# Optimization experiments

Hardware: AMD Instinct MI355X
Metric: run time of the kernel (lower is better)

## Reference

```python
import jax, jax.numpy as jnp
import numpy as np

NUM_HEADS = 16
NUM_HIDDENS = 1024
D_K = NUM_HIDDENS // NUM_HEADS
NEG_INF = -1.0e9


def setup_inputs() -> dict:
    key = jax.random.key(0)
    kx, kq, kk, kv, ko, kl = jax.random.split(key, 6)
    B, S, D = 2, 2048, NUM_HIDDENS
    scale = 1.0 / np.sqrt(D)
    return {
        "X": jax.random.normal(kx, (B, S, D), dtype=jnp.float32),
        "valid_lens": jax.random.randint(kl, (B,), 0, S, dtype=jnp.int64),
        "W_q": jax.random.normal(kq, (D, D), dtype=jnp.float32) * scale,
        "W_k": jax.random.normal(kk, (D, D), dtype=jnp.float32) * scale,
        "W_v": jax.random.normal(kv, (D, D), dtype=jnp.float32) * scale,
        "W_o": jax.random.normal(ko, (D, D), dtype=jnp.float32) * scale,
    }


def _split_heads(x):
    # [B, S, D] -> [B, H, S, d_k]
    B, S, _ = x.shape
    return x.reshape(B, S, NUM_HEADS, D_K).transpose(0, 2, 1, 3)


def reference(X, valid_lens, W_q, W_k, W_v, W_o):
    B, S, D = X.shape
    # nn.Linear(bias=False): y = x @ W.T  (W is [out, in])
    Q = _split_heads(jnp.einsum("bsd,ed->bse", X, W_q))  # [B,H,S,dk]
    K = _split_heads(jnp.einsum("bsd,ed->bse", X, W_k))
    V = _split_heads(jnp.einsum("bsd,ed->bse", X, W_v))

    scores = jnp.einsum("bhqd,bhkd->bhqk", Q, K) / jnp.sqrt(
        jnp.asarray(D_K, dtype=X.dtype)
    )  # [B,H,S,S]

    # key-position mask per batch: positions >= valid_len get -1e9
    mask = jnp.arange(S)[None, :] >= valid_lens[:, None]  # [B,S]
    scores = jnp.where(mask[:, None, None, :], jnp.asarray(NEG_INF, X.dtype), scores)

    attn = jax.nn.softmax(scores, axis=-1)  # dropout p=0 -> identity
    out = jnp.einsum("bhqk,bhkd->bhqd", attn, V)  # [B,H,S,dk]
    out = out.transpose(0, 2, 1, 3).reshape(B, S, D)
    return jnp.einsum("bsd,ed->bse", out, W_o)
```

## Files before the change

kernel.cpp:

```cpp
#include <hip/hip_runtime.h>
#include <stdint.h>

#define S_LEN 2048
#define BATCH 2
#define DMODEL 1024
#define NHEAD 16
#define DK 64
#define MROWS (BATCH * S_LEN)

typedef __attribute__((ext_vector_type(8))) short bf16x8;
typedef __attribute__((ext_vector_type(4))) float f32x4;
typedef __attribute__((ext_vector_type(4))) short short4v;
typedef __attribute__((ext_vector_type(2))) uint32_t u32x2;

__device__ __forceinline__ short f2b(float f) {
    union { float f; uint32_t u; } c; c.f = f;
    uint32_t u = c.u;
    return (short)((u + 0x7fffu + ((u >> 16) & 1u)) >> 16);
}

__device__ __forceinline__ void gload16(const void* g, void* l) {
    __builtin_amdgcn_global_load_lds(
        (const __attribute__((address_space(1))) void*)g,
        (__attribute__((address_space(3))) void*)l, 16, 0, 0);
}

__global__ void cvt_kernel(const float* __restrict__ X, const float* __restrict__ Wq,
                           const float* __restrict__ Wk, const float* __restrict__ Wv,
                           const float* __restrict__ Wo,
                           short* __restrict__ Xb, short* __restrict__ Wqb,
                           short* __restrict__ Wkb, short* __restrict__ Wvb,
                           short* __restrict__ Wob) {
    const float* src; short* dst; int n4;
    switch (blockIdx.y) {
        case 0:  src = X;  dst = Xb;  n4 = MROWS * DMODEL / 4;  break;
        case 1:  src = Wq; dst = Wqb; n4 = DMODEL * DMODEL / 4; break;
        case 2:  src = Wk; dst = Wkb; n4 = DMODEL * DMODEL / 4; break;
        case 3:  src = Wv; dst = Wvb; n4 = DMODEL * DMODEL / 4; break;
        default: src = Wo; dst = Wob; n4 = DMODEL * DMODEL / 4; break;
    }
    for (int i = blockIdx.x * blockDim.x + threadIdx.x; i < n4;
         i += gridDim.x * blockDim.x) {
        float4 v = ((const float4*)src)[i];
        short4v o;
        o[0] = f2b(v.x); o[1] = f2b(v.y); o[2] = f2b(v.z); o[3] = f2b(v.w);
        ((short4v*)dst)[i] = o;
    }
}

template <int OUT_F32>
__global__ __launch_bounds__(256) void gemm_bt(
    const short* __restrict__ A,
    const short* __restrict__ Bt0, const short* __restrict__ Bt1,
    const short* __restrict__ Bt2,
    short* __restrict__ Cb0, short* __restrict__ Cb1, short* __restrict__ Cb2,
    float* __restrict__ Cf, int M, int N, int K) {
    __shared__ short sA[2][128 * 32];
    __shared__ short sB[2][128 * 32];

    const short* Bt = Bt0;
    short* Cb = Cb0;
    if (blockIdx.z == 1) { Bt = Bt1; Cb = Cb1; }
    else if (blockIdx.z == 2) { Bt = Bt2; Cb = Cb2; }

    const int tid = threadIdx.x;
    const int lane = tid & 63;
    const int wid = tid >> 6;
    const int wr = wid >> 1, wc = wid & 1;
    const int brow = blockIdx.y * 128;
    const int bcol = blockIdx.x * 128;
    const int lr = lane & 15;
    const int kh = (lane >> 4) << 3;
    const int swg = ((lr >> 1) & 3) << 3;
    const int khs = kh ^ swg;

    f32x4 acc[4][4] = {};

    const int idx0 = tid, idx1 = tid + 256;
    const int ar0 = idx0 >> 2, ak0 = ((idx0 & 3) << 3) ^ (((ar0 >> 1) & 3) << 3);
    const int ar1 = idx1 >> 2, ak1 = ((idx1 & 3) << 3) ^ (((ar1 >> 1) & 3) << 3);

    const short* gA0 = A + (size_t)(brow + ar0) * K + ak0;
    const short* gA1 = A + (size_t)(brow + ar1) * K + ak1;
    const short* gB0 = Bt + (size_t)(bcol + ar0) * K + ak0;
    const short* gB1 = Bt + (size_t)(bcol + ar1) * K + ak1;

    const int nk = K >> 5;
    gload16(gA0, &sA[0][idx0 * 8]);
    gload16(gA1, &sA[0][idx1 * 8]);
    gload16(gB0, &sB[0][idx0 * 8]);
    gload16(gB1, &sB[0][idx1 * 8]);
    __syncthreads();

    int cur = 0;
    for (int kt = 0; kt < nk; ++kt) {
        if (kt + 1 < nk) {
            const int k0 = (kt + 1) << 5;
            gload16(gA0 + k0, &sA[cur ^ 1][idx0 * 8]);
            gload16(gA1 + k0, &sA[cur ^ 1][idx1 * 8]);
            gload16(gB0 + k0, &sB[cur ^ 1][idx0 * 8]);
            gload16(gB1 + k0, &sB[cur ^ 1][idx1 * 8]);
        }

        bf16x8 a[4], b[4];
#pragma unroll
        for (int mt = 0; mt < 4; ++mt)
            a[mt] = *(const bf16x8*)&sA[cur][(wr * 64 + mt * 16 + lr) * 32 + khs];
#pragma unroll
        for (int nt = 0; nt < 4; ++nt)
            b[nt] = *(const bf16x8*)&sB[cur][(wc * 64 + nt * 16 + lr) * 32 + khs];
        __builtin_amdgcn_s_setprio(1);
#pragma unroll
        for (int mt = 0; mt < 4; ++mt)
#pragma unroll
            for (int nt = 0; nt < 4; ++nt)
                acc[mt][nt] = __builtin_amdgcn_mfma_f32_16x16x32_bf16(
                    a[mt], b[nt], acc[mt][nt], 0, 0, 0);
        __builtin_amdgcn_s_setprio(0);

        __syncthreads();
        cur ^= 1;
    }

    const int rbase = (lane >> 4) << 2;
    const bool vtrans = (!OUT_F32) && (blockIdx.z == 2);
#pragma unroll
    for (int mt = 0; mt < 4; ++mt) {
#pragma unroll
        for (int nt = 0; nt < 4; ++nt) {
            if (vtrans) {
                int row0 = brow + wr * 64 + mt * 16 + rbase;
                int col = bcol + wc * 64 + nt * 16 + lr;
                int bb = row0 >> 11, key = row0 & 2047;
                int hh = col >> 6, d = col & 63;
                short4v pk;
#pragma unroll
                for (int j = 0; j < 4; ++j) pk[j] = f2b(acc[mt][nt][j]);
                *(short4v*)&Cb[((size_t)((bb * 16 + hh) * 64 + d)) * S_LEN + key] = pk;
            } else {
#pragma unroll
                for (int j = 0; j < 4; ++j) {
                    int row = brow + wr * 64 + mt * 16 + rbase + j;
                    int col = bcol + wc * 64 + nt * 16 + lr;
                    if (OUT_F32)
                        Cf[(size_t)row * N + col] = acc[mt][nt][j];
                    else
                        Cb[(size_t)row * N + col] = f2b(acc[mt][nt][j]);
                }
            }
        }
    }
}

__global__ __launch_bounds__(256) void attn_kernel(
    const short* __restrict__ Q, const short* __restrict__ K,
    const short* __restrict__ Vt, short* __restrict__ O,
    const int* __restrict__ vlens) {
    __shared__ short sK[2][64 * 64];
    __shared__ short sV[2][64 * 64];
    __shared__ short sP[4][2][16 * 64];

    const int tid = threadIdx.x;
    const int lane = tid & 63;
    const int w = tid >> 6;
    const int id = blockIdx.x;
    const int id2 = ((id & 7) << 6) | (id >> 3);
    const int qb = id2 & 15;
    const int bhx = id2 >> 4;
    const int b = bhx & 1, h = bhx >> 1;
    const int lr = lane & 15;
    const int kh = (lane >> 4) << 3;
    const int rbase = (lane >> 4) << 2;
    const int swq = (lr & 7) << 3;

    int vl = vlens[b];
    if (vl < 0) vl = 0;
    if (vl > S_LEN) vl = S_LEN;
    const bool allm = (vl == 0);
    if (allm) vl = S_LEN;
    const int nT = (vl + 63) >> 6;
    const int nFull = ((vl & 63) == 0) ? nT : nT - 1;

    const size_t rowbase = (size_t)(b * S_LEN) * DMODEL + h * DK;
    const short* vt = Vt + ((size_t)((b * 16 + h) * 64)) * S_LEN;

    const short* qrowA = Q + rowbase + (size_t)(qb * 128 + w * 32 + lr) * DMODEL;
    const short* qrowB = qrowA + 16 * DMODEL;
    bf16x8 qf0a = *(const bf16x8*)(qrowA + kh);
    bf16x8 qf1a = *(const bf16x8*)(qrowA + 32 + kh);
    bf16x8 qf0b = *(const bf16x8*)(qrowB + kh);
    bf16x8 qf1b = *(const bf16x8*)(qrowB + 32 + kh);
    if (allm) {
#pragma unroll
        for (int i = 0; i < 8; ++i) { qf0a[i] = 0; qf1a[i] = 0; qf0b[i] = 0; qf1b[i] = 0; }
    }

    f32x4 oacA[4] = {}, oacB[4] = {};
    float mA = -1e30f, mcA = -1e30f, lA = 0.f;
    float mB = -1e30f, mcB = -1e30f, lB = 0.f;
    const float CEXP = 0.18033688011112042f;
    const float THRADD = 44.361419556f;

    const int lofs0 = lr * 64 + (kh ^ swq);
    const int lofs1 = lr * 64 + ((32 + kh) ^ swq);

    const int kr0 = tid >> 3;
    const int kr1 = kr0 + 32;
    const int kc0 = (((tid & 7) ^ (kr0 & 7)) << 3);
    const int kc1 = (((tid & 7) ^ (kr1 & 7)) << 3);

    const short* kA = K + rowbase + (size_t)kr0 * DMODEL + kc0;
    const short* kB = K + rowbase + (size_t)kr1 * DMODEL + kc1;
    const short* vA = vt + (size_t)kr0 * S_LEN + kc0;
    const short* vB = vt + (size_t)kr1 * S_LEN + kc1;

    gload16(kA, &sK[0][tid * 8]);
    gload16(kB, &sK[0][(tid + 256) * 8]);
    gload16(vA, &sV[0][tid * 8]);
    gload16(vB, &sV[0][(tid + 256) * 8]);
    __syncthreads();

#define SOFTMAX_FRAG(SACC, MRUN, MC, LRUN, OAC, SPW)                            \
    do {                                                                        \
        float t0 = fmaxf(fmaxf(SACC[0][0], SACC[0][1]), SACC[0][2]);            \
        float t1 = fmaxf(fmaxf(SACC[0][3], SACC[1][0]), SACC[1][1]);            \
        float t2 = fmaxf(fmaxf(SACC[1][2], SACC[1][3]), SACC[2][0]);            \
        float t3 = fmaxf(fmaxf(SACC[2][1], SACC[2][2]), SACC[2][3]);            \
        float t4 = fmaxf(fmaxf(SACC[3][0], SACC[3][1]), SACC[3][2]);            \
        float pmax = fmaxf(fmaxf(fmaxf(t0, t1), t2),                            \
                           fmaxf(fmaxf(t3, t4), SACC[3][3]));                   \
        if (__any(pmax > MRUN + THRADD)) {                                      \
            float mx = pmax;                                                    \
            mx = fmaxf(mx, __shfl_xor(mx, 16));                                 \
            mx = fmaxf(mx, __shfl_xor(mx, 32));                                 \
            float scl = __builtin_exp2f((MRUN - mx) * CEXP);                    \
            MRUN = mx;                                                          \
            MC = mx * CEXP;                                                     \
            LRUN *= scl;                                                        \
            _Pragma("unroll")                                                   \
            for (int dt = 0; dt < 4; ++dt)                                      \
                _Pragma("unroll")                                               \
                for (int j = 0; j < 4; ++j) OAC[dt][j] *= scl;                  \
        }                                                                       \
        float p[16];                                                            \
        _Pragma("unroll")                                                       \
        for (int nt = 0; nt < 4; ++nt)                                          \
            _Pragma("unroll")                                                   \
            for (int j = 0; j < 4; ++j)                                         \
                p[nt * 4 + j] = __builtin_exp2f(                                \
                    __builtin_fmaf(SACC[nt][j], CEXP, -MC));                    \
        float ls = ((p[0] + p[1]) + (p[2] + p[3])) +                            \
                   ((p[4] + p[5]) + (p[6] + p[7]));                             \
        ls += ((p[8] + p[9]) + (p[10] + p[11])) +                               \
              ((p[12] + p[13]) + (p[14] + p[15]));                              \
        LRUN += ls;                                                             \
        _Pragma("unroll")                                                       \
        for (int nt = 0; nt < 4; ++nt) {                                        \
            u32x2 r;                                                            \
            asm("v_cvt_pk_bf16_f32 %0, %1, %2"                                  \
                : "=v"(r[0]) : "v"(p[nt * 4 + 0]), "v"(p[nt * 4 + 1]));         \
            asm("v_cvt_pk_bf16_f32 %0, %1, %2"                                  \
                : "=v"(r[1]) : "v"(p[nt * 4 + 2]), "v"(p[nt * 4 + 3]));         \
            *(u32x2*)&SPW[lr * 64 + ((nt * 16 + rbase) ^ swq)] = r;             \
        }                                                                       \
    } while (0)

#define TILE_BODY(MASKED_C)                                                     \
    do {                                                                        \
        constexpr bool MASKED = MASKED_C;                                       \
        const short* sKc = sK[cur];                                             \
        const short* sVc = sV[cur];                                             \
        const short* kL0 = sKc + lofs0;                                         \
        const short* kL1 = sKc + lofs1;                                         \
        f32x4 saccA[4] = {}, saccB[4] = {};                                     \
        __builtin_amdgcn_s_setprio(1);                                          \
        _Pragma("unroll")                                                       \
        for (int nt = 0; nt < 4; ++nt) {                                        \
            bf16x8 kb0 = *(const bf16x8*)&kL0[nt * 1024];                       \
            bf16x8 kb1 = *(const bf16x8*)&kL1[nt * 1024];                       \
            saccA[nt] = __builtin_amdgcn_mfma_f32_16x16x32_bf16(                \
                kb0, qf0a, saccA[nt], 0, 0, 0);                                 \
            saccB[nt] = __builtin_amdgcn_mfma_f32_16x16x32_bf16(                \
                kb0, qf0b, saccB[nt], 0, 0, 0);                                 \
            saccA[nt] = __builtin_amdgcn_mfma_f32_16x16x32_bf16(                \
                kb1, qf1a, saccA[nt], 0, 0, 0);                                 \
            saccB[nt] = __builtin_amdgcn_mfma_f32_16x16x32_bf16(                \
                kb1, qf1b, saccB[nt], 0, 0, 0);                                 \
        }                                                                       \
        __builtin_amdgcn_s_setprio(0);                                          \
        if (MASKED) {                                                           \
            _Pragma("unroll")                                                   \
            for (int nt = 0; nt < 4; ++nt)                                      \
                _Pragma("unroll")                                               \
                for (int j = 0; j < 4; ++j) {                                   \
                    int keyi = t * 64 + nt * 16 + rbase + j;                    \
                    if (keyi >= vl) { saccA[nt][j] = -3.0e38f;                  \
                                      saccB[nt][j] = -3.0e38f; }                \
                }                                                               \
        }                                                                       \
        SOFTMAX_FRAG(saccA, mA, mcA, lA, oacA, (&sP[w][0][0]));                 \
        SOFTMAX_FRAG(saccB, mB, mcB, lB, oacB, (&sP[w][1][0]));                 \
        const short* vL0 = sVc + lofs0;                                         \
        const short* vL1 = sVc + lofs1;                                         \
        __builtin_amdgcn_s_setprio(1);                                          \
        {                                                                       \
            bf16x8 pfA = *(const bf16x8*)&sP[w][0][lofs0];                      \
            bf16x8 pfB = *(const bf16x8*)&sP[w][1][lofs0];                      \
            _Pragma("unroll")                                                   \
            for (int dt = 0; dt < 4; ++dt) {                                    \
                bf16x8 vf = *(const bf16x8*)&vL0[dt * 1024];                    \
                oacA[dt] = __builtin_amdgcn_mfma_f32_16x16x32_bf16(             \
                    vf, pfA, oacA[dt], 0, 0, 0);                                \
                oacB[dt] = __builtin_amdgcn_mfma_f32_16x16x32_bf16(             \
                    vf, pfB, oacB[dt], 0, 0, 0);                                \
            }                                                                   \
            pfA = *(const bf16x8*)&sP[w][0][lofs1];                             \
            pfB = *(const bf16x8*)&sP[w][1][lofs1];                             \
            _Pragma("unroll")                                                   \
            for (int dt = 0; dt < 4; ++dt) {                                    \
                bf16x8 vf = *(const bf16x8*)&vL1[dt * 1024];                    \
                oacA[dt] = __builtin_amdgcn_mfma_f32_16x16x32_bf16(             \
                    vf, pfA, oacA[dt], 0, 0, 0);                                \
                oacB[dt] = __builtin_amdgcn_mfma_f32_16x16x32_bf16(             \
                    vf, pfB, oacB[dt], 0, 0, 0);                                \
            }                                                                   \
        }                                                                       \
        __builtin_amdgcn_s_setprio(0);                                          \
    } while (0)

    int cur = 0;
    for (int t = 0; t < nT; ++t) {
        const bool hn = (t + 1 < nT);
        if (hn) {
            short* sKn = sK[cur ^ 1];
            short* sVn = sV[cur ^ 1];
            kA += 64 * DMODEL; kB += 64 * DMODEL;
            vA += 64; vB += 64;
            gload16(kA, &sKn[tid * 8]);
            gload16(kB, &sKn[(tid + 256) * 8]);
            gload16(vA, &sVn[tid * 8]);
            gload16(vB, &sVn[(tid + 256) * 8]);
        }

        if (t < nFull) TILE_BODY(false);
        else TILE_BODY(true);

        __syncthreads();
        cur ^= 1;
    }
#undef TILE_BODY
#undef SOFTMAX_FRAG

    float ltA = lA + __shfl_xor(lA, 16);
    ltA += __shfl_xor(ltA, 32);
    float rlA = 1.f / ltA;
    float ltB = lB + __shfl_xor(lB, 16);
    ltB += __shfl_xor(ltB, 32);
    float rlB = 1.f / ltB;

    short* orowA = O + rowbase + (size_t)(qb * 128 + w * 32 + lr) * DMODEL;
    short* orowB = orowA + 16 * DMODEL;
#pragma unroll
    for (int dt = 0; dt < 4; ++dt) {
        short4v pkA, pkB;
#pragma unroll
        for (int j = 0; j < 4; ++j) {
            pkA[j] = f2b(oacA[dt][j] * rlA);
            pkB[j] = f2b(oacB[dt][j] * rlB);
        }
        *(short4v*)&orowA[dt * 16 + rbase] = pkA;
        *(short4v*)&orowB[dt * 16 + rbase] = pkB;
    }
}

extern "C" void kernel_launch(void* const* d_in, const int* in_sizes, int n_in,
                              void* d_out, int out_size, void* d_ws, size_t ws_size,
                              hipStream_t stream) {
    const float* X = (const float*)d_in[0];
    const int* vlens = (const int*)d_in[1];
    const float* Wq = (const float*)d_in[2];
    const float* Wk = (const float*)d_in[3];
    const float* Wv = (const float*)d_in[4];
    const float* Wo = (const float*)d_in[5];
    float* out = (float*)d_out;

    short* Xb = (short*)d_ws;
    short* Wqb = Xb + (size_t)MROWS * DMODEL;
    short* Wkb = Wqb + (size_t)DMODEL * DMODEL;
    short* Wvb = Wkb + (size_t)DMODEL * DMODEL;
    short* Wob = Wvb + (size_t)DMODEL * DMODEL;
    short* Qb = Wob + (size_t)DMODEL * DMODEL;
    short* Kb = Qb + (size_t)MROWS * DMODEL;
    short* Vtb = Kb + (size_t)MROWS * DMODEL;
    short* Ob = Vtb + (size_t)MROWS * DMODEL;

    cvt_kernel<<<dim3(512, 5), 256, 0, stream>>>(X, Wq, Wk, Wv, Wo, Xb, Wqb, Wkb,
                                                 Wvb, Wob);
    gemm_bt<0><<<dim3(8, 32, 3), 256, 0, stream>>>(Xb, Wqb, Wkb, Wvb, Qb, Kb, Vtb,
                                                   nullptr, MROWS, DMODEL, DMODEL);
    attn_kernel<<<dim3(512), 256, 0, stream>>>(Qb, Kb, Vtb, Ob, vlens);
    gemm_bt<1><<<dim3(8, 32, 1), 256, 0, stream>>>(Ob, Wob, Wob, Wob, nullptr,
                                                   nullptr, nullptr, out, MROWS,
                                                   DMODEL, DMODEL);
}
```

Before: 107.1 us.

## Halve attention block to 64 query rows with 2 waves, doubling grid size

The attention kernel now uses 128-thread blocks covering 64 query rows each instead of 256 threads covering 128, launching 1024 blocks instead of 512. The block-index swizzle, the K/V tile load loop and the P scratch buffer are resized to match. The aim is more blocks per CU and better load balance across the MI355X's CUs, especially since masked batches have uneven work. The cost is that each K/V tile loaded into LDS is shared by fewer query rows, so global and LDS traffic per unit of compute roughly doubles.

```diff
diff --git a/kernel.cpp b/kernel.cpp
--- a/kernel.cpp
+++ b/kernel.cpp
@@ -152,21 +152,21 @@
     }
 }
 
-__global__ __launch_bounds__(256) void attn_kernel(
+__global__ __launch_bounds__(128, 4) void attn_kernel(
     const short* __restrict__ Q, const short* __restrict__ K,
     const short* __restrict__ Vt, short* __restrict__ O,
     const int* __restrict__ vlens) {
     __shared__ short sK[2][64 * 64];
     __shared__ short sV[2][64 * 64];
-    __shared__ short sP[4][2][16 * 64];
+    __shared__ short sP[2][2][16 * 64];
 
     const int tid = threadIdx.x;
     const int lane = tid & 63;
     const int w = tid >> 6;
     const int id = blockIdx.x;
-    const int id2 = ((id & 7) << 6) | (id >> 3);
-    const int qb = id2 & 15;
-    const int bhx = id2 >> 4;
+    const int id2 = ((id & 7) << 7) | (id >> 3);
+    const int qb = id2 & 31;
+    const int bhx = id2 >> 5;
     const int b = bhx & 1, h = bhx >> 1;
     const int lr = lane & 15;
     const int kh = (lane >> 4) << 3;
@@ -184,7 +184,7 @@
     const size_t rowbase = (size_t)(b * S_LEN) * DMODEL + h * DK;
     const short* vt = Vt + ((size_t)((b * 16 + h) * 64)) * S_LEN;
 
-    const short* qrowA = Q + rowbase + (size_t)(qb * 128 + w * 32 + lr) * DMODEL;
+    const short* qrowA = Q + rowbase + (size_t)(qb * 64 + w * 32 + lr) * DMODEL;
     const short* qrowB = qrowA + 16 * DMODEL;
     bf16x8 qf0a = *(const bf16x8*)(qrowA + kh);
     bf16x8 qf1a = *(const bf16x8*)(qrowA + 32 + kh);
@@ -204,20 +204,16 @@
     const int lofs0 = lr * 64 + (kh ^ swq);
     const int lofs1 = lr * 64 + ((32 + kh) ^ swq);
 
-    const int kr0 = tid >> 3;
-    const int kr1 = kr0 + 32;
-    const int kc0 = (((tid & 7) ^ (kr0 & 7)) << 3);
-    const int kc1 = (((tid & 7) ^ (kr1 & 7)) << 3);
-
-    const short* kA = K + rowbase + (size_t)kr0 * DMODEL + kc0;
-    const short* kB = K + rowbase + (size_t)kr1 * DMODEL + kc1;
-    const short* vA = vt + (size_t)kr0 * S_LEN + kc0;
-    const short* vB = vt + (size_t)kr1 * S_LEN + kc1;
-
-    gload16(kA, &sK[0][tid * 8]);
-    gload16(kB, &sK[0][(tid + 256) * 8]);
-    gload16(vA, &sV[0][tid * 8]);
-    gload16(vB, &sV[0][(tid + 256) * 8]);
+    const int r0 = tid >> 3;
+    const int kc = (((tid & 7) ^ (r0 & 7)) << 3);
+    const short* kP = K + rowbase + (size_t)r0 * DMODEL + kc;
+    const short* vP = vt + (size_t)r0 * S_LEN + kc;
+
+#pragma unroll
+    for (int i = 0; i < 4; ++i) {
+        gload16(kP + (size_t)(i * 16) * DMODEL, &sK[0][(tid + i * 128) * 8]);
+        gload16(vP + (size_t)(i * 16) * S_LEN, &sV[0][(tid + i * 128) * 8]);
+    }
     __syncthreads();
 
 #define SOFTMAX_FRAG(SACC, MRUN, MC, LRUN, OAC, SPW)                            \
@@ -334,12 +330,13 @@
         if (hn) {
             short* sKn = sK[cur ^ 1];
             short* sVn = sV[cur ^ 1];
-            kA += 64 * DMODEL; kB += 64 * DMODEL;
-            vA += 64; vB += 64;
-            gload16(kA, &sKn[tid * 8]);
-            gload16(kB, &sKn[(tid + 256) * 8]);
-            gload16(vA, &sVn[tid * 8]);
-            gload16(vB, &sVn[(tid + 256) * 8]);
+            kP += 64 * DMODEL;
+            vP += 64;
+#pragma unroll
+            for (int i = 0; i < 4; ++i) {
+                gload16(kP + (size_t)(i * 16) * DMODEL, &sKn[(tid + i * 128) * 8]);
+                gload16(vP + (size_t)(i * 16) * S_LEN, &sVn[(tid + i * 128) * 8]);
+            }
         }
 
         if (t < nFull) TILE_BODY(false);
@@ -358,7 +355,7 @@
     ltB += __shfl_xor(ltB, 32);
     float rlB = 1.f / ltB;
 
-    short* orowA = O + rowbase + (size_t)(qb * 128 + w * 32 + lr) * DMODEL;
+    short* orowA = O + rowbase + (size_t)(qb * 64 + w * 32 + lr) * DMODEL;
     short* orowB = orowA + 16 * DMODEL;
 #pragma unroll
     for (int dt = 0; dt < 4; ++dt) {
@@ -398,7 +395,7 @@
                                                  Wvb, Wob);
     gemm_bt<0><<<dim3(8, 32, 3), 256, 0, stream>>>(Xb, Wqb, Wkb, Wvb, Qb, Kb, Vtb,
                                                    nullptr, MROWS, DMODEL, DMODEL);
-    attn_kernel<<<dim3(512), 256, 0, stream>>>(Qb, Kb, Vtb, Ob, vlens);
+    attn_kernel<<<dim3(1024), 128, 0, stream>>>(Qb, Kb, Vtb, Ob, vlens);
     gemm_bt<1><<<dim3(8, 32, 1), 256, 0, stream>>>(Ob, Wob, Wob, Wob, nullptr,
                                                    nullptr, nullptr, out, MROWS,
                                                    DMODEL, DMODEL);
```

After: 107.4 us. No clear change (+0.2%).
